# Performance work log

Measured on AMD Instinct MI355X. Metric: run time of the kernel, lower is better.

The kernel has to match this reference:

```python
import jax, jax.numpy as jnp
import numpy as np

D_MODEL = 1024
N_HEAD = 16
HEAD_DIM = D_MODEL // N_HEAD


def setup_inputs() -> dict:
    key = jax.random.key(0)
    ks = jax.random.split(key, 8)
    B, T, C = 4, 2048, D_MODEL
    scale = 1.0 / np.sqrt(C)
    return {
        "q": jax.random.normal(ks[0], (B, T, C), dtype=jnp.float32),
        "k": jax.random.normal(ks[1], (B, T, C), dtype=jnp.float32),
        "v": jax.random.normal(ks[2], (B, T, C), dtype=jnp.float32),
        # torch.nn.Linear weights are (out_features, in_features)
        "Wq": jax.random.normal(ks[3], (C, C), dtype=jnp.float32) * scale,
        "Wk": jax.random.normal(ks[4], (C, C), dtype=jnp.float32) * scale,
        "Wv": jax.random.normal(ks[5], (C, C), dtype=jnp.float32) * scale,
        "Wo": jax.random.normal(ks[6], (C, C), dtype=jnp.float32) * scale,
        "bo": jax.random.normal(ks[7], (C,), dtype=jnp.float32) * scale,
    }


def reference(q, k, v, Wq, Wk, Wv, Wo, bo):
    B, T, C = q.shape
    # projections (torch Linear: x @ W.T), split into heads -> (B, H, T, Dh)
    def split_heads(x, W):
        y = jnp.einsum('btc,oc->bto', x, W)
        return y.reshape(B, T, N_HEAD, HEAD_DIM).transpose(0, 2, 1, 3)

    qh = split_heads(q, Wq)
    kh = split_heads(k, Wk)
    vh = split_heads(v, Wv)

    # scaled dot-product attention with full T x T scores (as in source)
    scores = jnp.einsum('bhqd,bhkd->bhqk', qh, kh) / jnp.sqrt(
        jnp.asarray(HEAD_DIM, dtype=qh.dtype))
    attn = jax.nn.softmax(scores, axis=-1)
    out = jnp.einsum('bhqk,bhkd->bhqd', attn, vh)

    out = out.transpose(0, 2, 1, 3).reshape(B, T, C)
    # output projection (with bias); dropout is identity in eval mode
    return jnp.einsum('btc,oc->bto', out, Wo) + bo
```

## Files before the change

### kernel.cpp

```cpp
#include <hip/hip_runtime.h>

#define TSEQ  2048
#define NB    4
#define CDIM  1024
#define NHEAD 16
#define DH    64
#define MROWS (NB*TSEQ)

using bf16x8 = __attribute__((ext_vector_type(8))) __bf16;
using f32x4  = __attribute__((ext_vector_type(4))) float;
using u16x8  = __attribute__((ext_vector_type(8))) unsigned short;

__device__ __forceinline__ unsigned short f2bf(float x) {
  unsigned u = __float_as_uint(x);
  u += 0x7fffu + ((u >> 16) & 1u);
  return (unsigned short)(u >> 16);
}

__device__ __forceinline__ unsigned pkp(float lo, float hi) {
  return __builtin_amdgcn_perm(__float_as_uint(hi), __float_as_uint(lo), 0x07060302u);
}

__device__ __forceinline__ float fexp2(float x) {
  float r;
  asm("v_exp_f32 %0, %1" : "=v"(r) : "v"(x));
  return r;
}

__device__ __forceinline__ void gload_lds16(const void* g, void* l) {
  __builtin_amdgcn_global_load_lds(
      (const __attribute__((address_space(1))) void*)g,
      (__attribute__((address_space(3))) void*)l,
      16, 0, 0);
}

__global__ void cast3_f32_bf16(const float* __restrict__ a, const float* __restrict__ b,
                               const float* __restrict__ c, unsigned short* __restrict__ out,
                               int n) {
  const float* src = (blockIdx.y == 0) ? a : (blockIdx.y == 1) ? b : c;
  int i = (blockIdx.x * 256 + threadIdx.x) * 8;
  if (i >= n) return;
  float4 x = *(const float4*)(src + i);
  float4 y = *(const float4*)(src + i + 4);
  u16x8 r;
  r[0] = f2bf(x.x); r[1] = f2bf(x.y); r[2] = f2bf(x.z); r[3] = f2bf(x.w);
  r[4] = f2bf(y.x); r[5] = f2bf(y.y); r[6] = f2bf(y.z); r[7] = f2bf(y.w);
  *(u16x8*)(out + (size_t)blockIdx.y * n + i) = r;
}

__global__ void cast4_f32_bf16(const float* __restrict__ a, const float* __restrict__ b,
                               const float* __restrict__ c, const float* __restrict__ d,
                               unsigned short* __restrict__ out, int n) {
  const float* src = (blockIdx.y == 0) ? a : (blockIdx.y == 1) ? b
                   : (blockIdx.y == 2) ? c : d;
  int i = (blockIdx.x * 256 + threadIdx.x) * 8;
  if (i >= n) return;
  float4 x = *(const float4*)(src + i);
  float4 y = *(const float4*)(src + i + 4);
  u16x8 r;
  r[0] = f2bf(x.x); r[1] = f2bf(x.y); r[2] = f2bf(x.z); r[3] = f2bf(x.w);
  r[4] = f2bf(y.x); r[5] = f2bf(y.y); r[6] = f2bf(y.z); r[7] = f2bf(y.w);
  *(u16x8*)(out + (size_t)blockIdx.y * n + i) = r;
}

template<int MODE>
__global__ __launch_bounds__(256)
void gemm_bt(const unsigned short* __restrict__ A,
             const unsigned short* __restrict__ Bw,
             void* __restrict__ Cout,
             const float* __restrict__ bias,
             float qscale)
{
  constexpr int K  = CDIM;
  constexpr int BK = 64;
  __shared__ __attribute__((aligned(16))) unsigned short As[128 * BK];
  __shared__ __attribute__((aligned(16))) unsigned short Bs[128 * BK];

  const int tid = threadIdx.x;
  const int l   = tid & 63, w = tid >> 6;
  const int l16 = l & 15,  lq = l >> 4;
  const int wm  = w >> 1,  wn = w & 1;

  const int pz = (MODE == 0) ? blockIdx.z : 0;
  A  += (size_t)pz * MROWS * CDIM;
  Bw += (size_t)pz * CDIM * CDIM;
  const float oscale = (MODE == 0 && pz == 0) ? qscale : 1.0f;

  const int nwg  = gridDim.x * gridDim.y;
  const int orig = blockIdx.y * gridDim.x + blockIdx.x;
  const int wg   = (orig & 7) * (nwg >> 3) + (orig >> 3);
  const int m0   = (wg / gridDim.x) * 128, n0 = (wg % gridDim.x) * 128;

  f32x4 acc[4][4] = {};

  int srow[4], scol[4];
#pragma unroll
  for (int i = 0; i < 4; ++i) {
    int r = (i * 256 + tid) >> 3;
    srow[i] = r;
    scol[i] = (((tid & 7) ^ (r & 7)) << 3);
  }

  for (int kt = 0; kt < K; kt += BK) {
#pragma unroll
    for (int i = 0; i < 4; ++i) {
      gload_lds16(A  + (size_t)(m0 + srow[i]) * K + kt + scol[i],
                  (char*)As + (i * 256 + w * 64) * 16);
      gload_lds16(Bw + (size_t)(n0 + srow[i]) * K + kt + scol[i],
                  (char*)Bs + (i * 256 + w * 64) * 16);
    }
    __syncthreads();

#pragma unroll
    for (int kk = 0; kk < 2; ++kk) {
      bf16x8 af[4], bfr[4];
#pragma unroll
      for (int mi = 0; mi < 4; ++mi) {
        int row = wm * 64 + mi * 16 + l16;
        af[mi] = *(const bf16x8*)&As[row * BK + (((kk * 4 + lq) ^ (row & 7)) << 3)];
      }
#pragma unroll
      for (int nj = 0; nj < 4; ++nj) {
        int row = wn * 64 + nj * 16 + l16;
        bfr[nj] = *(const bf16x8*)&Bs[row * BK + (((kk * 4 + lq) ^ (row & 7)) << 3)];
      }
#pragma unroll
      for (int mi = 0; mi < 4; ++mi)
#pragma unroll
        for (int nj = 0; nj < 4; ++nj)
          acc[mi][nj] = __builtin_amdgcn_mfma_f32_16x16x32_bf16(af[mi], bfr[nj], acc[mi][nj], 0, 0, 0);
    }
    __syncthreads();
  }

#pragma unroll
  for (int mi = 0; mi < 4; ++mi) {
#pragma unroll
    for (int nj = 0; nj < 4; ++nj) {
      int gn = n0 + wn * 64 + nj * 16 + l16;
#pragma unroll
      for (int r = 0; r < 4; ++r) {
        int gm = m0 + wm * 64 + mi * 16 + lq * 4 + r;
        float v = acc[mi][nj][r];
        if constexpr (MODE == 0) {
          int b = gm >> 11, t = gm & (TSEQ - 1);
          int h = gn >> 6,  d = gn & 63;
          ((unsigned short*)Cout)[(size_t)pz * MROWS * CDIM +
              ((((size_t)b * NHEAD + h) * TSEQ + t) << 6) + d] = f2bf(v * oscale);
        } else {
          ((float*)Cout)[(size_t)gm * CDIM + gn] = v + bias[gn];
        }
      }
    }
  }
}

__global__ __launch_bounds__(256)
void attn_fwd(const unsigned short* __restrict__ Qh,
              const unsigned short* __restrict__ Kh,
              const unsigned short* __restrict__ Vh,
              unsigned short* __restrict__ O)
{
  __shared__ __attribute__((aligned(16))) unsigned short Ks[2][64 * DH];
  __shared__ __attribute__((aligned(16))) unsigned short Vt[2][DH * 64];

  const int tid = threadIdx.x;
  const int l   = tid & 63, w = tid >> 6;
  const int l16 = l & 15,  lq = l >> 4;

  const int orig    = blockIdx.y * gridDim.x + blockIdx.x;
  const int logical = (orig & 7) * 128 + (orig >> 3);
  const int bh  = logical >> 4;
  const int q0  = (logical & 15) * 128;
  const size_t base = (size_t)bh * TSEQ * DH;

  bf16x8 qfA0, qfA1, qfB0, qfB1;
  {
    const unsigned short* qp = Qh + base + (size_t)(q0 + w * 32 + l16) * DH + lq * 8;
    qfA0 = *(const bf16x8*)qp;
    qfA1 = *(const bf16x8*)(qp + 32);
    qfB0 = *(const bf16x8*)(qp + 16 * DH);
    qfB1 = *(const bf16x8*)(qp + 16 * DH + 32);
  }

  union { unsigned short u[8]; bf16x8 v; } onesu;
#pragma unroll
  for (int i = 0; i < 8; ++i) onesu.u[i] = 0x3F80;
  const bf16x8 ones = onesu.v;

  f32x4 oaccA[4] = {}, oaccB[4] = {};
  f32x4 laccA = {}, laccB = {};

  const int vc  = tid & 7;
  const int vu  = tid >> 3;
  const int kva = ((vu >> 4) << 5) | (vu & 15);
  const int vslot = ((vu >> 4) << 5) | (((vu >> 2) & 3) << 3) |
                    ((vu & 1) << 2) | (((vu >> 1) & 1) << 1);

  constexpr int TILE_STRIDE = 64 * DH;
  const int krow = tid >> 3;
  const int kcol = ((tid & 7) ^ (krow & 7)) << 3;
  const unsigned short* kPtr = Kh + base + (size_t)krow * DH + kcol;
  const unsigned short* vPtr = Vh + base + (size_t)kva * DH + vc * 8;

  auto stageK = [&](int bb) {
    gload_lds16(kPtr,                  (char*)Ks[bb] + (w * 64) * 16);
    gload_lds16(kPtr + 32 * DH,        (char*)Ks[bb] + (256 + w * 64) * 16);
  };
  auto loadV = [&](u16x8& v0, u16x8& v1) {
    v0 = *(const u16x8*)vPtr;
    v1 = *(const u16x8*)(vPtr + 16 * DH);
  };
  auto writeV = [&](int bb, u16x8 v0, u16x8 v1) {
    union { u16x8 v; unsigned u[4]; } a, b;
    a.v = v0; b.v = v1;
#pragma unroll
    for (int r = 0; r < 4; ++r) {
      unsigned w0 = __builtin_amdgcn_perm(b.u[r], a.u[r], 0x05040100u);
      unsigned w1 = __builtin_amdgcn_perm(b.u[r], a.u[r], 0x07060302u);
      int d0 = vc * 8 + 2 * r;
      int a0 = ((d0 << 7) + (vslot << 1)) ^ ((((d0 & 7) ^ (d0 >> 3)) & 7) << 4);
      int d1 = d0 + 1;
      int a1 = ((d1 << 7) + (vslot << 1)) ^ ((((d1 & 7) ^ (d1 >> 3)) & 7) << 4);
      *(unsigned*)((char*)Vt[bb] + a0) = w0;
      *(unsigned*)((char*)Vt[bb] + a1) = w1;
    }
  };

  {
    u16x8 v0, v1;
    loadV(v0, v1);
    stageK(0);
    writeV(0, v0, v1);
    kPtr += TILE_STRIDE;
    vPtr += TILE_STRIDE;
  }
  __syncthreads();

  constexpr int NT = TSEQ / 64;

  auto iter = [&](int t, int bb) {
    const bool hasNext = (t + 1 < NT);
    u16x8 nv0, nv1;
    if (hasNext) {
      loadV(nv0, nv1);
      stageK(bb ^ 1);
      kPtr += TILE_STRIDE;
      vPtr += TILE_STRIDE;
    }

    f32x4 sA[4] = {}, sB[4] = {};
#pragma unroll
    for (int nj = 0; nj < 4; ++nj) {
      int row = nj * 16 + l16;
      bf16x8 kf0 = *(const bf16x8*)&Ks[bb][row * DH + ((lq ^ (row & 7)) << 3)];
      bf16x8 kf1 = *(const bf16x8*)&Ks[bb][row * DH + (((4 + lq) ^ (row & 7)) << 3)];
      sA[nj] = __builtin_amdgcn_mfma_f32_16x16x32_bf16(kf0, qfA0, sA[nj], 0, 0, 0);
      sA[nj] = __builtin_amdgcn_mfma_f32_16x16x32_bf16(kf1, qfA1, sA[nj], 0, 0, 0);
      sB[nj] = __builtin_amdgcn_mfma_f32_16x16x32_bf16(kf0, qfB0, sB[nj], 0, 0, 0);
      sB[nj] = __builtin_amdgcn_mfma_f32_16x16x32_bf16(kf1, qfB1, sB[nj], 0, 0, 0);
    }

#pragma unroll
    for (int nj = 0; nj < 4; ++nj)
#pragma unroll
      for (int r = 0; r < 4; ++r) {
        sA[nj][r] = fexp2(sA[nj][r]);
        sB[nj][r] = fexp2(sB[nj][r]);
      }

    union { unsigned d[4]; bf16x8 v; } pA0, pA1, pB0, pB1;
    pA0.d[0] = pkp(sA[0][0], sA[1][0]); pA0.d[1] = pkp(sA[0][2], sA[1][2]);
    pA0.d[2] = pkp(sA[0][1], sA[1][1]); pA0.d[3] = pkp(sA[0][3], sA[1][3]);
    pA1.d[0] = pkp(sA[2][0], sA[3][0]); pA1.d[1] = pkp(sA[2][2], sA[3][2]);
    pA1.d[2] = pkp(sA[2][1], sA[3][1]); pA1.d[3] = pkp(sA[2][3], sA[3][3]);
    pB0.d[0] = pkp(sB[0][0], sB[1][0]); pB0.d[1] = pkp(sB[0][2], sB[1][2]);
    pB0.d[2] = pkp(sB[0][1], sB[1][1]); pB0.d[3] = pkp(sB[0][3], sB[1][3]);
    pB1.d[0] = pkp(sB[2][0], sB[3][0]); pB1.d[1] = pkp(sB[2][2], sB[3][2]);
    pB1.d[2] = pkp(sB[2][1], sB[3][1]); pB1.d[3] = pkp(sB[2][3], sB[3][3]);

    laccA = __builtin_amdgcn_mfma_f32_16x16x32_bf16(pA0.v, ones, laccA, 0, 0, 0);
    laccA = __builtin_amdgcn_mfma_f32_16x16x32_bf16(pA1.v, ones, laccA, 0, 0, 0);
    laccB = __builtin_amdgcn_mfma_f32_16x16x32_bf16(pB0.v, ones, laccB, 0, 0, 0);
    laccB = __builtin_amdgcn_mfma_f32_16x16x32_bf16(pB1.v, ones, laccB, 0, 0, 0);

    if (hasNext) writeV(bb ^ 1, nv0, nv1);

#pragma unroll
    for (int dj = 0; dj < 4; ++dj) {
      int d  = dj * 16 + l16;
      int cx = ((((d & 7) ^ (d >> 3)) & 7) << 4);
#pragma unroll
      for (int c = 0; c < 2; ++c) {
        int byteaddr = (((d << 6) + (c << 5) + (lq << 3)) << 1) ^ cx;
        bf16x8 vf = *(const bf16x8*)((const char*)Vt[bb] + byteaddr);
        oaccA[dj] = __builtin_amdgcn_mfma_f32_16x16x32_bf16(c ? pA1.v : pA0.v, vf, oaccA[dj], 0, 0, 0);
        oaccB[dj] = __builtin_amdgcn_mfma_f32_16x16x32_bf16(c ? pB1.v : pB0.v, vf, oaccB[dj], 0, 0, 0);
      }
    }
    __syncthreads();
  };

  for (int tt = 0; tt < NT; tt += 2) {
    iter(tt, 0);
    iter(tt + 1, 1);
  }

  const int b = bh >> 4, h = bh & (NHEAD - 1);
#pragma unroll
  for (int r = 0; r < 4; ++r) {
    float invA = 1.f / laccA[r];
    float invB = 1.f / laccB[r];
    size_t obA = ((size_t)b * TSEQ + (q0 + w * 32 + lq * 4 + r)) * CDIM + h * DH;
    size_t obB = obA + (size_t)16 * CDIM;
#pragma unroll
    for (int dj = 0; dj < 4; ++dj) {
      O[obA + dj * 16 + l16] = f2bf(oaccA[dj][r] * invA);
      O[obB + dj * 16 + l16] = f2bf(oaccB[dj][r] * invB);
    }
  }
}

extern "C" void kernel_launch(void* const* d_in, const int* in_sizes, int n_in,
                              void* d_out, int out_size, void* d_ws, size_t ws_size,
                              hipStream_t stream) {
  const float* q  = (const float*)d_in[0];
  const float* k  = (const float*)d_in[1];
  const float* v  = (const float*)d_in[2];
  const float* Wq = (const float*)d_in[3];
  const float* Wk = (const float*)d_in[4];
  const float* Wv = (const float*)d_in[5];
  const float* Wo = (const float*)d_in[6];
  const float* bo = (const float*)d_in[7];

  char* ws = (char*)d_ws;
  const size_t SZ_ACT = (size_t)MROWS * CDIM * 2;
  const size_t SZ_W   = (size_t)CDIM * CDIM * 2;
  unsigned short* qb  = (unsigned short*)(ws);
  unsigned short* wqb = (unsigned short*)(ws + 3 * SZ_ACT);
  unsigned short* wob = (unsigned short*)(ws + 3 * SZ_ACT + 3 * SZ_W);
  unsigned short* Qh  = (unsigned short*)(ws + 3 * SZ_ACT + 4 * SZ_W);
  unsigned short* Kh  = (unsigned short*)(ws + 4 * SZ_ACT + 4 * SZ_W);
  unsigned short* Vh  = (unsigned short*)(ws + 5 * SZ_ACT + 4 * SZ_W);
  unsigned short* AttO = qb;

  const int nAct = MROWS * CDIM;
  const int nW   = CDIM * CDIM;

  cast3_f32_bf16<<<dim3(nAct / 2048, 3), 256, 0, stream>>>(q, k, v, qb, nAct);
  cast4_f32_bf16<<<dim3(nW / 2048, 4), 256, 0, stream>>>(Wq, Wk, Wv, Wo, wqb, nW);

  const float QSCALE = 0.18033688011112042f;

  gemm_bt<0><<<dim3(CDIM / 128, MROWS / 128, 3), 256, 0, stream>>>(
      qb, wqb, Qh, nullptr, QSCALE);

  attn_fwd<<<dim3(TSEQ / 128, NB * NHEAD), 256, 0, stream>>>(Qh, Kh, Vh, AttO);

  gemm_bt<1><<<dim3(CDIM / 128, MROWS / 128, 1), 256, 0, stream>>>(
      AttO, wob, (float*)d_out, bo, 1.0f);
}
```

Baseline: 201.6 us.

## Precompute LDS addresses, peel last iteration, add setprio and occupancy hint

Hoists the swizzled LDS address calculations for K reads, V transposed writes and PV reads into per-thread register arrays computed once, so the inner loop no longer repeats that integer arithmetic. The final tile iteration is peeled out so the prefetch branch becomes a compile-time constant. s_setprio is raised around the MFMA groups to favour matrix issue across waves, and launch bounds now request 3 waves per SIMD. The extra address registers may compete with the occupancy target and cause spills.

Result: faster. 192.6 us (-4.5%).

```diff
diff --git a/kernel.cpp b/kernel.cpp
--- a/kernel.cpp
+++ b/kernel.cpp
@@ -155,7 +155,7 @@
   }
 }
 
-__global__ __launch_bounds__(256)
+__global__ __launch_bounds__(256, 3)
 void attn_fwd(const unsigned short* __restrict__ Qh,
               const unsigned short* __restrict__ Kh,
               const unsigned short* __restrict__ Vh,
@@ -197,6 +197,28 @@
   const int vslot = ((vu >> 4) << 5) | (((vu >> 2) & 3) << 3) |
                     ((vu & 1) << 2) | (((vu >> 1) & 1) << 1);
 
+  int vAddr[8];
+#pragma unroll
+  for (int j = 0; j < 8; ++j) {
+    int d = vc * 8 + j;
+    vAddr[j] = ((d << 7) + (vslot << 1)) ^ ((((d & 7) ^ (d >> 3)) & 7) << 4);
+  }
+  int kAddr[8];
+#pragma unroll
+  for (int nj = 0; nj < 4; ++nj) {
+    int row = nj * 16 + l16;
+    kAddr[nj * 2 + 0] = (row << 7) + ((lq       ^ (row & 7)) << 4);
+    kAddr[nj * 2 + 1] = (row << 7) + (((4 + lq) ^ (row & 7)) << 4);
+  }
+  int pvAddr[8];
+#pragma unroll
+  for (int dj = 0; dj < 4; ++dj) {
+    int d  = dj * 16 + l16;
+    int cx = (((d & 7) ^ (d >> 3)) & 7) << 4;
+    pvAddr[dj * 2 + 0] = (((d << 6) + (lq << 3)) << 1) ^ cx;
+    pvAddr[dj * 2 + 1] = (((d << 6) + 32 + (lq << 3)) << 1) ^ cx;
+  }
+
   constexpr int TILE_STRIDE = 64 * DH;
   const int krow = tid >> 3;
   const int kcol = ((tid & 7) ^ (krow & 7)) << 3;
@@ -204,8 +226,8 @@
   const unsigned short* vPtr = Vh + base + (size_t)kva * DH + vc * 8;
 
   auto stageK = [&](int bb) {
-    gload_lds16(kPtr,                  (char*)Ks[bb] + (w * 64) * 16);
-    gload_lds16(kPtr + 32 * DH,        (char*)Ks[bb] + (256 + w * 64) * 16);
+    gload_lds16(kPtr,           (char*)Ks + bb * 8192 + (w * 64) * 16);
+    gload_lds16(kPtr + 32 * DH, (char*)Ks + bb * 8192 + (256 + w * 64) * 16);
   };
   auto loadV = [&](u16x8& v0, u16x8& v1) {
     v0 = *(const u16x8*)vPtr;
@@ -214,16 +236,13 @@
   auto writeV = [&](int bb, u16x8 v0, u16x8 v1) {
     union { u16x8 v; unsigned u[4]; } a, b;
     a.v = v0; b.v = v1;
+    char* vb = (char*)Vt + bb * 8192;
 #pragma unroll
     for (int r = 0; r < 4; ++r) {
       unsigned w0 = __builtin_amdgcn_perm(b.u[r], a.u[r], 0x05040100u);
       unsigned w1 = __builtin_amdgcn_perm(b.u[r], a.u[r], 0x07060302u);
-      int d0 = vc * 8 + 2 * r;
-      int a0 = ((d0 << 7) + (vslot << 1)) ^ ((((d0 & 7) ^ (d0 >> 3)) & 7) << 4);
-      int d1 = d0 + 1;
-      int a1 = ((d1 << 7) + (vslot << 1)) ^ ((((d1 & 7) ^ (d1 >> 3)) & 7) << 4);
-      *(unsigned*)((char*)Vt[bb] + a0) = w0;
-      *(unsigned*)((char*)Vt[bb] + a1) = w1;
+      *(unsigned*)(vb + vAddr[2 * r])     = w0;
+      *(unsigned*)(vb + vAddr[2 * r + 1]) = w1;
     }
   };
 
@@ -239,10 +258,9 @@
 
   constexpr int NT = TSEQ / 64;
 
-  auto iter = [&](int t, int bb) {
-    const bool hasNext = (t + 1 < NT);
+  auto body = [&](int bb, bool PF) {
     u16x8 nv0, nv1;
-    if (hasNext) {
+    if (PF) {
       loadV(nv0, nv1);
       stageK(bb ^ 1);
       kPtr += TILE_STRIDE;
@@ -250,16 +268,17 @@
     }
 
     f32x4 sA[4] = {}, sB[4] = {};
+    __builtin_amdgcn_s_setprio(1);
 #pragma unroll
     for (int nj = 0; nj < 4; ++nj) {
-      int row = nj * 16 + l16;
-      bf16x8 kf0 = *(const bf16x8*)&Ks[bb][row * DH + ((lq ^ (row & 7)) << 3)];
-      bf16x8 kf1 = *(const bf16x8*)&Ks[bb][row * DH + (((4 + lq) ^ (row & 7)) << 3)];
+      bf16x8 kf0 = *(const bf16x8*)((const char*)Ks + bb * 8192 + kAddr[nj * 2 + 0]);
+      bf16x8 kf1 = *(const bf16x8*)((const char*)Ks + bb * 8192 + kAddr[nj * 2 + 1]);
       sA[nj] = __builtin_amdgcn_mfma_f32_16x16x32_bf16(kf0, qfA0, sA[nj], 0, 0, 0);
       sA[nj] = __builtin_amdgcn_mfma_f32_16x16x32_bf16(kf1, qfA1, sA[nj], 0, 0, 0);
       sB[nj] = __builtin_amdgcn_mfma_f32_16x16x32_bf16(kf0, qfB0, sB[nj], 0, 0, 0);
       sB[nj] = __builtin_amdgcn_mfma_f32_16x16x32_bf16(kf1, qfB1, sB[nj], 0, 0, 0);
     }
+    __builtin_amdgcn_s_setprio(0);
 
 #pragma unroll
     for (int nj = 0; nj < 4; ++nj)
@@ -279,32 +298,35 @@
     pB1.d[0] = pkp(sB[2][0], sB[3][0]); pB1.d[1] = pkp(sB[2][2], sB[3][2]);
     pB1.d[2] = pkp(sB[2][1], sB[3][1]); pB1.d[3] = pkp(sB[2][3], sB[3][3]);
 
+    __builtin_amdgcn_s_setprio(1);
     laccA = __builtin_amdgcn_mfma_f32_16x16x32_bf16(pA0.v, ones, laccA, 0, 0, 0);
     laccA = __builtin_amdgcn_mfma_f32_16x16x32_bf16(pA1.v, ones, laccA, 0, 0, 0);
     laccB = __builtin_amdgcn_mfma_f32_16x16x32_bf16(pB0.v, ones, laccB, 0, 0, 0);
     laccB = __builtin_amdgcn_mfma_f32_16x16x32_bf16(pB1.v, ones, laccB, 0, 0, 0);
-
-    if (hasNext) writeV(bb ^ 1, nv0, nv1);
-
+    __builtin_amdgcn_s_setprio(0);
+
+    if (PF) writeV(bb ^ 1, nv0, nv1);
+
+    __builtin_amdgcn_s_setprio(1);
 #pragma unroll
     for (int dj = 0; dj < 4; ++dj) {
-      int d  = dj * 16 + l16;
-      int cx = ((((d & 7) ^ (d >> 3)) & 7) << 4);
 #pragma unroll
       for (int c = 0; c < 2; ++c) {
-        int byteaddr = (((d << 6) + (c << 5) + (lq << 3)) << 1) ^ cx;
-        bf16x8 vf = *(const bf16x8*)((const char*)Vt[bb] + byteaddr);
+        bf16x8 vf = *(const bf16x8*)((const char*)Vt + bb * 8192 + pvAddr[dj * 2 + c]);
         oaccA[dj] = __builtin_amdgcn_mfma_f32_16x16x32_bf16(c ? pA1.v : pA0.v, vf, oaccA[dj], 0, 0, 0);
         oaccB[dj] = __builtin_amdgcn_mfma_f32_16x16x32_bf16(c ? pB1.v : pB0.v, vf, oaccB[dj], 0, 0, 0);
       }
     }
+    __builtin_amdgcn_s_setprio(0);
     __syncthreads();
   };
 
-  for (int tt = 0; tt < NT; tt += 2) {
-    iter(tt, 0);
-    iter(tt + 1, 1);
-  }
+  for (int tt = 0; tt < NT - 2; tt += 2) {
+    body(0, true);
+    body(1, true);
+  }
+  body(0, true);
+  body(1, false);
 
   const int b = bh >> 4, h = bh & (NHEAD - 1);
 #pragma unroll
```
